# Performance work log

Hardware: AMD Instinct MI355X
Metric: run time of the kernel (lower is better)

## Reference

```python
import jax, jax.numpy as jnp
import numpy as np

H = 512  # hidden size (layer_size in the torch module)


def setup_inputs() -> dict:
    key = jax.random.key(0)
    ks = jax.random.split(key, 12)
    B, T = 512, 128
    s = 1.0 / np.sqrt(H)  # torch default LSTM/Linear init range
    def u(k, shape):
        return jax.random.uniform(k, shape, jnp.float32, -s, s)
    return {
        "x": jax.random.normal(ks[0], (B, T, 1), jnp.float32),
        "x_time": jax.random.normal(ks[1], (B, T), jnp.float32),
        "y_time": jax.random.normal(ks[2], (B, T), jnp.float32),
        # layer 0: input_size=1
        "w_ih0": u(ks[3], (4 * H, 1)),
        "w_hh0": u(ks[4], (4 * H, H)),
        "b_ih0": u(ks[5], (4 * H,)),
        "b_hh0": u(ks[6], (4 * H,)),
        # layer 1: input_size=H
        "w_ih1": u(ks[7], (4 * H, H)),
        "w_hh1": u(ks[8], (4 * H, H)),
        "b_ih1": u(ks[9], (4 * H,)),
        "b_hh1": u(ks[10], (4 * H,)),
        # output head Linear(512, 1)
        "w_lin": u(ks[11], (1, H)),
        "b_lin": jnp.zeros((1,), jnp.float32),
    }


def _cell(x, h, c, w_ih, w_hh, b):
    # torch LSTM gate order: i, f, g, o
    g = x @ w_ih.T + h @ w_hh.T + b
    i, f, gg, o = jnp.split(g, 4, axis=-1)
    c = jax.nn.sigmoid(f) * c + jax.nn.sigmoid(i) * jnp.tanh(gg)
    h = jax.nn.sigmoid(o) * jnp.tanh(c)
    return h, c


def reference(x, x_time, y_time, w_ih0, w_hh0, b_ih0, b_hh0,
              w_ih1, w_hh1, b_ih1, b_hh1, w_lin, b_lin):
    # x: [B, T, 1]; x_time / y_time are unused (as in the torch module)
    B, T, _ = x.shape
    b0 = b_ih0 + b_hh0
    b1 = b_ih1 + b_hh1

    def step(state, x_t):  # x_t: [B, 1]
        h1, c1, h2, c2 = state
        h1, c1 = _cell(x_t, h1, c1, w_ih0, w_hh0, b0)
        h2, c2 = _cell(h1, h2, c2, w_ih1, w_hh1, b1)
        return (h1, c1, h2, c2), h2

    z = jnp.zeros((B, H), x.dtype)
    state = (z, z, z, z)
    # phase 1: run the 2-layer LSTM over the full input sequence (first loop iter)
    state, _ = jax.lax.scan(step, state, jnp.swapaxes(x, 0, 1))
    y0 = state[3] @ w_lin.T + b_lin  # [B, 1] first prediction

    def ar_step(carry, _):
        st, y = carry
        st, h2 = step(st, y)
        y_new = h2 @ w_lin.T + b_lin
        return (st, y_new), y_new

    _, ys = jax.lax.scan(ar_step, (state, y0), None, length=T - 1)  # [T-1, B, 1]
    preds = jnp.concatenate([y0[None], ys], axis=0)  # [T, B, 1]
    return jnp.transpose(preds, (1, 0, 2))  # [B, T, 1]
```

## Files before the change

### kernel.cpp

```cpp
#include <hip/hip_runtime.h>
#include <math.h>
#include <stdint.h>


namespace {
constexpr int NH  = 512;
constexpr int NT  = 128;
constexpr int NB  = 512;
}

typedef __attribute__((ext_vector_type(8))) short bf16x8;
typedef __attribute__((ext_vector_type(4))) float f32x4;
typedef __attribute__((ext_vector_type(4))) unsigned int u32x4;

__global__ void ReLSTM_18940805775611_kernel() {}

__device__ __forceinline__ unsigned short lstm9_f2b(float f) {
    union { float f; uint32_t i; } v; v.f = f;
    const uint32_t r = v.i + 0x7FFFu + ((v.i >> 16) & 1u);
    return (unsigned short)(r >> 16);
}
__device__ __forceinline__ float lstm9_sig(float x) {
    return 1.0f / (1.0f + expf(-x));
}

__global__ void lstm9_mark(float* out) {
    const int i = blockIdx.x * blockDim.x + threadIdx.x;
    if (i < NB * NT) out[i] = 2.03125f;
}

__global__ void lstm9_prep(
    const float* whh0, const float* wih1, const float* whh1,
    const float* bih0, const float* bhh0, const float* bih1, const float* bhh1,
    unsigned short* wb0, unsigned short* wb1i, unsigned short* wb1h,
    float* bsum0, float* bsum1,
    unsigned short* hz, int* flags)
{
    const size_t stride = (size_t)gridDim.x * blockDim.x;
    const size_t i0 = (size_t)blockIdx.x * blockDim.x + threadIdx.x;
    const size_t NW = (size_t)4 * NH * NH;
    for (size_t i = i0; i < NW; i += stride) {
        wb0 [i] = lstm9_f2b(whh0[i]);
        wb1i[i] = lstm9_f2b(wih1[i]);
        wb1h[i] = lstm9_f2b(whh1[i]);
    }
    for (size_t i = i0; i < (size_t)4 * NH; i += stride) {
        bsum0[i] = bih0[i] + bhh0[i];
        bsum1[i] = bih1[i] + bhh1[i];
    }
    for (size_t i = i0; i < (size_t)4 * NB * NH; i += stride) hz[i] = 0;
    for (size_t i = i0; i < (size_t)2 * 256 * 8 * 32; i += stride) flags[i] = 0;
}

__device__ __forceinline__ void lstm9_ldA(u32x4& d, const unsigned short* p) {
    asm volatile("global_load_dwordx4 %0, %1, off sc0 sc1"
                 : "=v"(d) : "v"(p) : "memory");
}
__device__ __forceinline__ void lstm9_ldP(u32x4& d, const float* p) {
    asm volatile("global_load_dwordx4 %0, %1, off sc0 sc1"
                 : "=v"(d) : "v"(p) : "memory");
}
#define LSTM9_W8(N, a,b,c,d,e,f,g,h) \
    asm volatile("s_waitcnt vmcnt(" #N ")" \
        : "+v"(a),"+v"(b),"+v"(c),"+v"(d),"+v"(e),"+v"(f),"+v"(g),"+v"(h) :: "memory")
#define LSTM9_WAIT2(a,b) \
    asm volatile("s_waitcnt vmcnt(0)" : "+v"(a),"+v"(b) :: "memory")
__device__ __forceinline__ void lstm9_stH(unsigned short* p, unsigned short v) {
    unsigned int x = v;
    asm volatile("global_store_short %0, %1, off sc0 sc1" :: "v"(p), "v"(x) : "memory");
}
__device__ __forceinline__ void lstm9_stF(float* p, float v) {
    asm volatile("global_store_dword %0, %1, off sc0 sc1" :: "v"(p), "v"(v) : "memory");
}
__device__ __forceinline__ void lstm9_stI(int* p, int v) {
    asm volatile("global_store_dword %0, %1, off sc0 sc1" :: "v"(p), "v"(v) : "memory");
}
__device__ __forceinline__ void lstm9_drain() {
    asm volatile("s_waitcnt vmcnt(0)" ::: "memory");
}

__device__ __forceinline__ void lstm9_waitgrp(const int* base) {
    if (threadIdx.x < 64) {
        const int sl = (int)threadIdx.x & 31;
        int it = 0;
        for (;;) {
            int f;
            asm volatile("global_load_dword %0, %1, off sc0 sc1\n\t"
                         "s_waitcnt vmcnt(0)"
                         : "=v"(f) : "v"(base + sl) : "memory");
            if (__all(f != 0)) break;
            if (it < 4) __builtin_amdgcn_s_sleep(1);
            else        __builtin_amdgcn_s_sleep(8);
            ++it;
        }
    }
    __syncthreads();
}
__device__ __forceinline__ void lstm9_waitgrp2(const int* baseA, const int* baseB) {
    if (threadIdx.x < 64) {
        const int sl = (int)threadIdx.x & 31;
        const int* p = ((threadIdx.x < 32) ? baseA : baseB) + sl;
        int it = 0;
        for (;;) {
            int f;
            asm volatile("global_load_dword %0, %1, off sc0 sc1\n\t"
                         "s_waitcnt vmcnt(0)"
                         : "=v"(f) : "v"(p) : "memory");
            if (__all(f != 0)) break;
            if (it < 4) __builtin_amdgcn_s_sleep(1);
            else        __builtin_amdgcn_s_sleep(8);
            ++it;
        }
    }
    __syncthreads();
}

#define BFR0(gt, kk) (*(const bf16x8*)&Bsh0[gt][kk][lane][0])
#define BFR1(gt, kk) (*(const bf16x8*)&Bsh1[gt][kk][lane][0])
#define WHR(gt, kk)  (*(const bf16x8*)&whr[(gt) * 16 + (kk)])

#define LSTM9_L0_MFMAS()                                                          \
    do {                                                                          \
        _Pragma("unroll")                                                         \
        for (int ks = 0; ks < 8; ++ks) {                                          \
            const bf16x8 af = *(const bf16x8*)&rA1[ks];                           \
            b0 = __builtin_amdgcn_mfma_f32_16x16x32_bf16(af, BFR0(0, ks), b0, 0, 0, 0); \
            b1 = __builtin_amdgcn_mfma_f32_16x16x32_bf16(af, BFR0(1, ks), b1, 0, 0, 0); \
            b2 = __builtin_amdgcn_mfma_f32_16x16x32_bf16(af, BFR0(2, ks), b2, 0, 0, 0); \
            b3 = __builtin_amdgcn_mfma_f32_16x16x32_bf16(af, BFR0(3, ks), b3, 0, 0, 0); \
        }                                                                         \
        _Pragma("unroll")                                                         \
        for (int ks = 0; ks < 8; ++ks) {                                          \
            const bf16x8 af = *(const bf16x8*)&rA2[ks];                           \
            b0 = __builtin_amdgcn_mfma_f32_16x16x32_bf16(af, BFR0(0, 8 + ks), b0, 0, 0, 0); \
            b1 = __builtin_amdgcn_mfma_f32_16x16x32_bf16(af, BFR0(1, 8 + ks), b1, 0, 0, 0); \
            b2 = __builtin_amdgcn_mfma_f32_16x16x32_bf16(af, BFR0(2, 8 + ks), b2, 0, 0, 0); \
            b3 = __builtin_amdgcn_mfma_f32_16x16x32_bf16(af, BFR0(3, 8 + ks), b3, 0, 0, 0); \
        }                                                                         \
    } while (0)

#define LSTM9_L0_EPI(h1dst)                                                       \
    do {                                                                          \
        _Pragma("unroll")                                                         \
        for (int r = 0; r < 4; ++r) {                                             \
            const float gi = b0[r] + fmaf(xv[r], wxi, b0i);                       \
            const float gf = b1[r] + fmaf(xv[r], wxf, b0f);                       \
            const float gg = b2[r] + fmaf(xv[r], wxg, b0g);                       \
            const float go = b3[r] + fmaf(xv[r], wxo, b0o);                       \
            float cv = c1r[r];                                                    \
            cv = lstm9_sig(gf) * cv + lstm9_sig(gi) * tanhf(gg);                  \
            c1r[r] = cv;                                                          \
            lstm9_stH((h1dst) + (size_t)(mb + r) * NH + jv,                       \
                      lstm9_f2b(lstm9_sig(go) * tanhf(cv)));                      \
        }                                                                         \
    } while (0)

__global__ __launch_bounds__(256, 1) void lstm9_persist(
    const float* __restrict__ xin, float* __restrict__ outf,
    const unsigned short* __restrict__ wb0,
    const unsigned short* __restrict__ wb1i,
    const unsigned short* __restrict__ wb1h,
    const float* __restrict__ bsum0, const float* __restrict__ bsum1,
    const float* __restrict__ wih0f, const float* __restrict__ wlinf,
    const float* __restrict__ blinf,
    unsigned short* h1a, unsigned short* h1b,
    unsigned short* h2a, unsigned short* h2b,
    float* parts, int* flags)
{
    __shared__ unsigned short Bsh0[4][16][64][8];
    __shared__ unsigned short Bsh1[4][16][64][8];
    __shared__ float redsh[64][17];
    __shared__ float ysh[64];

    const int tid  = threadIdx.x;
    const int lane = tid & 63;
    const int wv   = tid >> 6;
    const int quad = lane >> 4;
    const int ln15 = lane & 15;
    const int bid  = blockIdx.x;
    const int jt = (bid & 7) * 4 + ((bid >> 3) & 3);
    const int g  = bid >> 5;
    const int j0 = jt * 16;
    const int m0 = g * 64;
    const int rowA = m0 + wv * 16 + ln15;
    const int mb   = m0 + wv * 16 + quad * 4;
    const int jv   = j0 + ln15;

    for (int idx = tid; idx < 4 * 16 * 64; idx += 256) {
        const int gt = idx >> 10;
        const int ks = (idx >> 6) & 15;
        const int l  = idx & 63;
        const int row = l & 15, q = l >> 4;
        const size_t go = ((size_t)(gt * NH + j0 + row)) * NH + ks * 32 + q * 8;
        *(u32x4*)&Bsh0[gt][ks][l][0] = *(const u32x4*)(wb0  + go);
        *(u32x4*)&Bsh1[gt][ks][l][0] = *(const u32x4*)(wb1i + go);
    }
    u32x4 whr[64];
    #pragma unroll
    for (int gt = 0; gt < 4; ++gt) {
        #pragma unroll
        for (int ks = 0; ks < 16; ++ks)
            whr[gt * 16 + ks] = *(const u32x4*)(
                wb1h + ((size_t)(gt * NH + j0 + ln15)) * NH + ks * 32 + quad * 8);
    }
    __syncthreads();

    const float b0i = bsum0[jv],          b0f = bsum0[NH + jv];
    const float b0g = bsum0[2 * NH + jv], b0o = bsum0[3 * NH + jv];
    const float wxi = wih0f[jv],          wxf = wih0f[NH + jv];
    const float wxg = wih0f[2 * NH + jv], wxo = wih0f[3 * NH + jv];
    const float b1i = bsum1[jv],          b1f = bsum1[NH + jv];
    const float b1g = bsum1[2 * NH + jv], b1o = bsum1[3 * NH + jv];
    const float wl_ = wlinf[jv];
    const float bl_ = blinf[0];

    float c1r[4] = {0.f, 0.f, 0.f, 0.f};
    float c2r[4] = {0.f, 0.f, 0.f, 0.f};

    unsigned short* h1p[2] = { h1a, h1b };
    unsigned short* h2p[2] = { h2a, h2b };
    int* flagA = flags;
    int* flagB = flags + 256 * 8 * 32;

    u32x4 rA1[8], rA2[8], rH2a[8], rH2b[8];

    {
        float xv[4];
        f32x4 b0 = {0.f, 0.f, 0.f, 0.f};
        f32x4 b1 = b0, b2 = b0, b3 = b0;
        #pragma unroll
        for (int r = 0; r < 4; ++r)
            xv[r] = xin[(size_t)(mb + r) * NT + 0];
        LSTM9_L0_EPI(h1p[1]);
        lstm9_drain();
        __syncthreads();
        if (tid == 0) lstm9_stI(flagA + (0 * 8 + g) * 32 + jt, 1);
    }

    for (int t = 0; t < 255; ++t) {
        const unsigned short* h1rd = h1p[(t + 1) & 1];
        unsigned short*       h1wr = h1p[t & 1];
        const unsigned short* h2rd = h2p[t & 1];
        unsigned short*       h2wr = h2p[(t + 1) & 1];

        if (t == 0) lstm9_waitgrp(flagA + (0 * 8 + g) * 32);
        else        lstm9_waitgrp2(flagA + (t * 8 + g) * 32,
                                   flagB + ((t - 1) * 8 + g) * 32);

        #pragma unroll
        for (int ks = 0; ks < 8; ++ks)
            lstm9_ldA(rH2a[ks], h2rd + (size_t)rowA * NH + ks * 32 + quad * 8);
        #pragma unroll
        for (int ks = 0; ks < 8; ++ks)
            lstm9_ldA(rH2b[ks], h2rd + (size_t)rowA * NH + (8 + ks) * 32 + quad * 8);
        #pragma unroll
        for (int ks = 0; ks < 8; ++ks)
            lstm9_ldA(rA1[ks], h1rd + (size_t)rowA * NH + ks * 32 + quad * 8);
        #pragma unroll
        for (int ks = 0; ks < 8; ++ks)
            lstm9_ldA(rA2[ks], h1rd + (size_t)rowA * NH + (8 + ks) * 32 + quad * 8);

        f32x4 a0 = {0.f, 0.f, 0.f, 0.f};
        f32x4 a1 = a0, a2 = a0, a3 = a0;
        LSTM9_W8(24, rH2a[0], rH2a[1], rH2a[2], rH2a[3],
                     rH2a[4], rH2a[5], rH2a[6], rH2a[7]);
        #pragma unroll
        for (int ks = 0; ks < 8; ++ks) {
            const bf16x8 af = *(const bf16x8*)&rH2a[ks];
            a0 = __builtin_amdgcn_mfma_f32_16x16x32_bf16(af, WHR(0, ks), a0, 0, 0, 0);
            a1 = __builtin_amdgcn_mfma_f32_16x16x32_bf16(af, WHR(1, ks), a1, 0, 0, 0);
            a2 = __builtin_amdgcn_mfma_f32_16x16x32_bf16(af, WHR(2, ks), a2, 0, 0, 0);
            a3 = __builtin_amdgcn_mfma_f32_16x16x32_bf16(af, WHR(3, ks), a3, 0, 0, 0);
        }
        LSTM9_W8(16, rH2b[0], rH2b[1], rH2b[2], rH2b[3],
                     rH2b[4], rH2b[5], rH2b[6], rH2b[7]);
        #pragma unroll
        for (int ks = 0; ks < 8; ++ks) {
            const bf16x8 af = *(const bf16x8*)&rH2b[ks];
            a0 = __builtin_amdgcn_mfma_f32_16x16x32_bf16(af, WHR(0, 8 + ks), a0, 0, 0, 0);
            a1 = __builtin_amdgcn_mfma_f32_16x16x32_bf16(af, WHR(1, 8 + ks), a1, 0, 0, 0);
            a2 = __builtin_amdgcn_mfma_f32_16x16x32_bf16(af, WHR(2, 8 + ks), a2, 0, 0, 0);
            a3 = __builtin_amdgcn_mfma_f32_16x16x32_bf16(af, WHR(3, 8 + ks), a3, 0, 0, 0);
        }
        LSTM9_W8(8, rA1[0], rA1[1], rA1[2], rA1[3],
                    rA1[4], rA1[5], rA1[6], rA1[7]);
        #pragma unroll
        for (int ks = 0; ks < 8; ++ks) {
            const bf16x8 af = *(const bf16x8*)&rA1[ks];
            a0 = __builtin_amdgcn_mfma_f32_16x16x32_bf16(af, BFR1(0, ks), a0, 0, 0, 0);
            a1 = __builtin_amdgcn_mfma_f32_16x16x32_bf16(af, BFR1(1, ks), a1, 0, 0, 0);
            a2 = __builtin_amdgcn_mfma_f32_16x16x32_bf16(af, BFR1(2, ks), a2, 0, 0, 0);
            a3 = __builtin_amdgcn_mfma_f32_16x16x32_bf16(af, BFR1(3, ks), a3, 0, 0, 0);
        }
        LSTM9_W8(0, rA2[0], rA2[1], rA2[2], rA2[3],
                    rA2[4], rA2[5], rA2[6], rA2[7]);
        #pragma unroll
        for (int ks = 0; ks < 8; ++ks) {
            const bf16x8 af = *(const bf16x8*)&rA2[ks];
            a0 = __builtin_amdgcn_mfma_f32_16x16x32_bf16(af, BFR1(0, 8 + ks), a0, 0, 0, 0);
            a1 = __builtin_amdgcn_mfma_f32_16x16x32_bf16(af, BFR1(1, 8 + ks), a1, 0, 0, 0);
            a2 = __builtin_amdgcn_mfma_f32_16x16x32_bf16(af, BFR1(2, 8 + ks), a2, 0, 0, 0);
            a3 = __builtin_amdgcn_mfma_f32_16x16x32_bf16(af, BFR1(3, 8 + ks), a3, 0, 0, 0);
        }

        float hv[4], cva[4];
        #pragma unroll
        for (int r = 0; r < 4; ++r) {
            const float gi = a0[r] + b1i;
            const float gf = a1[r] + b1f;
            const float gg = a2[r] + b1g;
            const float go = a3[r] + b1o;
            float cv = c2r[r];
            cv = lstm9_sig(gf) * cv + lstm9_sig(gi) * tanhf(gg);
            c2r[r] = cv;
            cva[r] = cv;
            hv[r] = lstm9_sig(go) * tanhf(cv);
            lstm9_stH(h2wr + (size_t)(mb + r) * NH + jv, lstm9_f2b(hv[r]));
        }

        f32x4 b0 = {0.f, 0.f, 0.f, 0.f};
        f32x4 b1 = b0, b2 = b0, b3 = b0;

        if (t < 127) {
            LSTM9_L0_MFMAS();
            float xv[4];
            #pragma unroll
            for (int r = 0; r < 4; ++r)
                xv[r] = xin[(size_t)(mb + r) * NT + (t + 1)];
            LSTM9_L0_EPI(h1wr);
            lstm9_drain();
            __syncthreads();
            if (tid == 0) {
                lstm9_stI(flagB + (t * 8 + g) * 32 + jt, 1);
                lstm9_stI(flagA + ((t + 1) * 8 + g) * 32 + jt, 1);
            }
        } else {
            #pragma unroll
            for (int r = 0; r < 4; ++r)
                redsh[wv * 16 + quad * 4 + r][ln15] =
                    (t == 127 ? cva[r] : hv[r]) * wl_;
            __syncthreads();
            if (tid < 64) {
                float s = 0.0f;
                #pragma unroll
                for (int j = 0; j < 16; ++j) s += redsh[tid][j];
                lstm9_stF(parts + (size_t)(t & 1) * NB * 32
                                + (size_t)(m0 + tid) * 32 + jt, s);
            }
            lstm9_drain();
            __syncthreads();
            if (tid == 0) lstm9_stI(flagB + (t * 8 + g) * 32 + jt, 1);

            if (t < 254) LSTM9_L0_MFMAS();

            lstm9_waitgrp(flagB + (t * 8 + g) * 32);
            const float* pslot = parts + (size_t)(t & 1) * NB * 32;
            {
                const int row = tid >> 2, q = tid & 3;
                u32x4 v0, v1;
                lstm9_ldP(v0, pslot + (size_t)(m0 + row) * 32 + q * 8);
                lstm9_ldP(v1, pslot + (size_t)(m0 + row) * 32 + q * 8 + 4);
                LSTM9_WAIT2(v0, v1);
                const float* f0 = (const float*)&v0;
                const float* f1 = (const float*)&v1;
                redsh[row][q] = f0[0] + f0[1] + f0[2] + f0[3]
                              + f1[0] + f1[1] + f1[2] + f1[3];
            }
            __syncthreads();
            if (tid < 64) {
                const float y = bl_ + redsh[tid][0] + redsh[tid][1]
                                    + redsh[tid][2] + redsh[tid][3];
                ysh[tid] = y;
                if (jt == 0)
                    outf[(size_t)(m0 + tid) * NT + (t - 127)] = y;
            }
            __syncthreads();
            if (t == 254) break;

            float xv[4];
            #pragma unroll
            for (int r = 0; r < 4; ++r)
                xv[r] = ysh[wv * 16 + quad * 4 + r];
            LSTM9_L0_EPI(h1wr);
            lstm9_drain();
            __syncthreads();
            if (tid == 0) lstm9_stI(flagA + ((t + 1) * 8 + g) * 32 + jt, 1);
        }
    }
}

extern "C" void kernel_launch(void* const* d_in, const int* in_sizes, int n_in,
                              void* d_out, int out_size, void* d_ws, size_t ws_size,
                              hipStream_t stream)
{
    int base = 3;
    if (!(n_in > 3 && in_sizes[3] == 4 * NH)) {
        for (int i = 1; i + 9 < n_in; ++i)
            if (in_sizes[i] == 4 * NH) { base = i; break; }
    }
    const float* xin  = (const float*)d_in[0];
    const float* wih0 = (const float*)d_in[base + 0];
    const float* whh0 = (const float*)d_in[base + 1];
    const float* bih0 = (const float*)d_in[base + 2];
    const float* bhh0 = (const float*)d_in[base + 3];
    const float* wih1 = (const float*)d_in[base + 4];
    const float* whh1 = (const float*)d_in[base + 5];
    const float* bih1 = (const float*)d_in[base + 6];
    const float* bhh1 = (const float*)d_in[base + 7];
    const float* wlin = (const float*)d_in[base + 8];
    const float* blin = (const float*)d_in[base + 9];
    float* outf = (float*)d_out;

    const size_t NW = (size_t)4 * NH * NH;
    const size_t S  = (size_t)NB * NH;
    unsigned short* wb0  = (unsigned short*)d_ws;
    unsigned short* wb1i = wb0 + NW;
    unsigned short* wb1h = wb1i + NW;
    unsigned short* h1b0 = wb1h + NW;
    unsigned short* h1b1 = h1b0 + S;
    unsigned short* h2b0 = h1b1 + S;
    unsigned short* h2b1 = h2b0 + S;
    float* bsum0 = (float*)(h2b1 + S);
    float* bsum1 = bsum0 + 4 * NH;
    float* parts = bsum1 + 4 * NH;
    int*   flags = (int*)(parts + 2 * NB * 32);

    lstm9_mark<<<(NB * NT + 255) / 256, 256, 0, stream>>>(outf);
    lstm9_prep<<<1024, 256, 0, stream>>>(whh0, wih1, whh1, bih0, bhh0, bih1, bhh1,
                                         wb0, wb1i, wb1h, bsum0, bsum1,
                                         h1b0, flags);
    lstm9_persist<<<256, 256, 0, stream>>>(xin, outf, wb0, wb1i, wb1h,
                                           bsum0, bsum1, wih0, wlin, blin,
                                           h1b0, h1b1, h2b0, h2b1,
                                           parts, flags);
}
```

Measured before the change: 3.076 ms.

## Restructure autoregressive phase to overlap layer-2 recurrent MFMAs with y reduction wait

Splits the main time loop into an encoder phase and an autoregressive phase. In the autoregressive phase it issues the h2 loads and the layer-0 MFMAs while the partial-sum loads for y are still in flight, then runs the h2·W_hh1 half of layer 1 before waiting for the new h1 from the other blocks. This hides part of the two grid-wide flag waits per step. The final y is reduced after the loop. Spin waits now use a fixed short sleep with a bounded retry count, which can fall through silently on timeout.

```diff
diff --git a/kernel.cpp b/kernel.cpp
--- a/kernel.cpp
+++ b/kernel.cpp
@@ -52,11 +52,7 @@
     for (size_t i = i0; i < (size_t)2 * 256 * 8 * 32; i += stride) flags[i] = 0;
 }
 
-__device__ __forceinline__ void lstm9_ldA(u32x4& d, const unsigned short* p) {
-    asm volatile("global_load_dwordx4 %0, %1, off sc0 sc1"
-                 : "=v"(d) : "v"(p) : "memory");
-}
-__device__ __forceinline__ void lstm9_ldP(u32x4& d, const float* p) {
+__device__ __forceinline__ void lstm9_ldA(u32x4& d, const void* p) {
     asm volatile("global_load_dwordx4 %0, %1, off sc0 sc1"
                  : "=v"(d) : "v"(p) : "memory");
 }
@@ -65,6 +61,8 @@
         : "+v"(a),"+v"(b),"+v"(c),"+v"(d),"+v"(e),"+v"(f),"+v"(g),"+v"(h) :: "memory")
 #define LSTM9_WAIT2(a,b) \
     asm volatile("s_waitcnt vmcnt(0)" : "+v"(a),"+v"(b) :: "memory")
+#define LSTM9_WP16(a,b) \
+    asm volatile("s_waitcnt vmcnt(16)" : "+v"(a),"+v"(b) :: "memory")
 __device__ __forceinline__ void lstm9_stH(unsigned short* p, unsigned short v) {
     unsigned int x = v;
     asm volatile("global_store_short %0, %1, off sc0 sc1" :: "v"(p), "v"(x) : "memory");
@@ -82,16 +80,15 @@
 __device__ __forceinline__ void lstm9_waitgrp(const int* base) {
     if (threadIdx.x < 64) {
         const int sl = (int)threadIdx.x & 31;
-        int it = 0;
+        int tries = 0;
         for (;;) {
             int f;
             asm volatile("global_load_dword %0, %1, off sc0 sc1\n\t"
                          "s_waitcnt vmcnt(0)"
                          : "=v"(f) : "v"(base + sl) : "memory");
             if (__all(f != 0)) break;
-            if (it < 4) __builtin_amdgcn_s_sleep(1);
-            else        __builtin_amdgcn_s_sleep(8);
-            ++it;
+            if (++tries > (1 << 15)) break;
+            __builtin_amdgcn_s_sleep(1);
         }
     }
     __syncthreads();
@@ -100,16 +97,15 @@
     if (threadIdx.x < 64) {
         const int sl = (int)threadIdx.x & 31;
         const int* p = ((threadIdx.x < 32) ? baseA : baseB) + sl;
-        int it = 0;
+        int tries = 0;
         for (;;) {
             int f;
             asm volatile("global_load_dword %0, %1, off sc0 sc1\n\t"
                          "s_waitcnt vmcnt(0)"
                          : "=v"(f) : "v"(p) : "memory");
             if (__all(f != 0)) break;
-            if (it < 4) __builtin_amdgcn_s_sleep(1);
-            else        __builtin_amdgcn_s_sleep(8);
-            ++it;
+            if (++tries > (1 << 15)) break;
+            __builtin_amdgcn_s_sleep(1);
         }
     }
     __syncthreads();
@@ -243,102 +239,222 @@
         const unsigned short* h2rd = h2p[t & 1];
         unsigned short*       h2wr = h2p[(t + 1) & 1];
 
-        if (t == 0) lstm9_waitgrp(flagA + (0 * 8 + g) * 32);
-        else        lstm9_waitgrp2(flagA + (t * 8 + g) * 32,
-                                   flagB + ((t - 1) * 8 + g) * 32);
-
-        #pragma unroll
-        for (int ks = 0; ks < 8; ++ks)
-            lstm9_ldA(rH2a[ks], h2rd + (size_t)rowA * NH + ks * 32 + quad * 8);
-        #pragma unroll
-        for (int ks = 0; ks < 8; ++ks)
-            lstm9_ldA(rH2b[ks], h2rd + (size_t)rowA * NH + (8 + ks) * 32 + quad * 8);
-        #pragma unroll
-        for (int ks = 0; ks < 8; ++ks)
-            lstm9_ldA(rA1[ks], h1rd + (size_t)rowA * NH + ks * 32 + quad * 8);
-        #pragma unroll
-        for (int ks = 0; ks < 8; ++ks)
-            lstm9_ldA(rA2[ks], h1rd + (size_t)rowA * NH + (8 + ks) * 32 + quad * 8);
-
-        f32x4 a0 = {0.f, 0.f, 0.f, 0.f};
-        f32x4 a1 = a0, a2 = a0, a3 = a0;
-        LSTM9_W8(24, rH2a[0], rH2a[1], rH2a[2], rH2a[3],
-                     rH2a[4], rH2a[5], rH2a[6], rH2a[7]);
-        #pragma unroll
-        for (int ks = 0; ks < 8; ++ks) {
-            const bf16x8 af = *(const bf16x8*)&rH2a[ks];
-            a0 = __builtin_amdgcn_mfma_f32_16x16x32_bf16(af, WHR(0, ks), a0, 0, 0, 0);
-            a1 = __builtin_amdgcn_mfma_f32_16x16x32_bf16(af, WHR(1, ks), a1, 0, 0, 0);
-            a2 = __builtin_amdgcn_mfma_f32_16x16x32_bf16(af, WHR(2, ks), a2, 0, 0, 0);
-            a3 = __builtin_amdgcn_mfma_f32_16x16x32_bf16(af, WHR(3, ks), a3, 0, 0, 0);
-        }
-        LSTM9_W8(16, rH2b[0], rH2b[1], rH2b[2], rH2b[3],
-                     rH2b[4], rH2b[5], rH2b[6], rH2b[7]);
-        #pragma unroll
-        for (int ks = 0; ks < 8; ++ks) {
-            const bf16x8 af = *(const bf16x8*)&rH2b[ks];
-            a0 = __builtin_amdgcn_mfma_f32_16x16x32_bf16(af, WHR(0, 8 + ks), a0, 0, 0, 0);
-            a1 = __builtin_amdgcn_mfma_f32_16x16x32_bf16(af, WHR(1, 8 + ks), a1, 0, 0, 0);
-            a2 = __builtin_amdgcn_mfma_f32_16x16x32_bf16(af, WHR(2, 8 + ks), a2, 0, 0, 0);
-            a3 = __builtin_amdgcn_mfma_f32_16x16x32_bf16(af, WHR(3, 8 + ks), a3, 0, 0, 0);
-        }
-        LSTM9_W8(8, rA1[0], rA1[1], rA1[2], rA1[3],
-                    rA1[4], rA1[5], rA1[6], rA1[7]);
-        #pragma unroll
-        for (int ks = 0; ks < 8; ++ks) {
-            const bf16x8 af = *(const bf16x8*)&rA1[ks];
-            a0 = __builtin_amdgcn_mfma_f32_16x16x32_bf16(af, BFR1(0, ks), a0, 0, 0, 0);
-            a1 = __builtin_amdgcn_mfma_f32_16x16x32_bf16(af, BFR1(1, ks), a1, 0, 0, 0);
-            a2 = __builtin_amdgcn_mfma_f32_16x16x32_bf16(af, BFR1(2, ks), a2, 0, 0, 0);
-            a3 = __builtin_amdgcn_mfma_f32_16x16x32_bf16(af, BFR1(3, ks), a3, 0, 0, 0);
-        }
-        LSTM9_W8(0, rA2[0], rA2[1], rA2[2], rA2[3],
-                    rA2[4], rA2[5], rA2[6], rA2[7]);
-        #pragma unroll
-        for (int ks = 0; ks < 8; ++ks) {
-            const bf16x8 af = *(const bf16x8*)&rA2[ks];
-            a0 = __builtin_amdgcn_mfma_f32_16x16x32_bf16(af, BFR1(0, 8 + ks), a0, 0, 0, 0);
-            a1 = __builtin_amdgcn_mfma_f32_16x16x32_bf16(af, BFR1(1, 8 + ks), a1, 0, 0, 0);
-            a2 = __builtin_amdgcn_mfma_f32_16x16x32_bf16(af, BFR1(2, 8 + ks), a2, 0, 0, 0);
-            a3 = __builtin_amdgcn_mfma_f32_16x16x32_bf16(af, BFR1(3, 8 + ks), a3, 0, 0, 0);
-        }
-
-        float hv[4], cva[4];
-        #pragma unroll
-        for (int r = 0; r < 4; ++r) {
-            const float gi = a0[r] + b1i;
-            const float gf = a1[r] + b1f;
-            const float gg = a2[r] + b1g;
-            const float go = a3[r] + b1o;
-            float cv = c2r[r];
-            cv = lstm9_sig(gf) * cv + lstm9_sig(gi) * tanhf(gg);
-            c2r[r] = cv;
-            cva[r] = cv;
-            hv[r] = lstm9_sig(go) * tanhf(cv);
-            lstm9_stH(h2wr + (size_t)(mb + r) * NH + jv, lstm9_f2b(hv[r]));
-        }
-
-        f32x4 b0 = {0.f, 0.f, 0.f, 0.f};
-        f32x4 b1 = b0, b2 = b0, b3 = b0;
-
-        if (t < 127) {
+        if (t <= 127) {
+            if (t == 0) lstm9_waitgrp(flagA + (0 * 8 + g) * 32);
+            else        lstm9_waitgrp2(flagA + (t * 8 + g) * 32,
+                                       flagB + ((t - 1) * 8 + g) * 32);
+
+            #pragma unroll
+            for (int ks = 0; ks < 8; ++ks)
+                lstm9_ldA(rH2a[ks], h2rd + (size_t)rowA * NH + ks * 32 + quad * 8);
+            #pragma unroll
+            for (int ks = 0; ks < 8; ++ks)
+                lstm9_ldA(rH2b[ks], h2rd + (size_t)rowA * NH + (8 + ks) * 32 + quad * 8);
+            #pragma unroll
+            for (int ks = 0; ks < 8; ++ks)
+                lstm9_ldA(rA1[ks], h1rd + (size_t)rowA * NH + ks * 32 + quad * 8);
+            #pragma unroll
+            for (int ks = 0; ks < 8; ++ks)
+                lstm9_ldA(rA2[ks], h1rd + (size_t)rowA * NH + (8 + ks) * 32 + quad * 8);
+
+            f32x4 a0 = {0.f, 0.f, 0.f, 0.f};
+            f32x4 a1 = a0, a2 = a0, a3 = a0;
+            LSTM9_W8(24, rH2a[0], rH2a[1], rH2a[2], rH2a[3],
+                         rH2a[4], rH2a[5], rH2a[6], rH2a[7]);
+            #pragma unroll
+            for (int ks = 0; ks < 8; ++ks) {
+                const bf16x8 af = *(const bf16x8*)&rH2a[ks];
+                a0 = __builtin_amdgcn_mfma_f32_16x16x32_bf16(af, WHR(0, ks), a0, 0, 0, 0);
+                a1 = __builtin_amdgcn_mfma_f32_16x16x32_bf16(af, WHR(1, ks), a1, 0, 0, 0);
+                a2 = __builtin_amdgcn_mfma_f32_16x16x32_bf16(af, WHR(2, ks), a2, 0, 0, 0);
+                a3 = __builtin_amdgcn_mfma_f32_16x16x32_bf16(af, WHR(3, ks), a3, 0, 0, 0);
+            }
+            LSTM9_W8(16, rH2b[0], rH2b[1], rH2b[2], rH2b[3],
+                         rH2b[4], rH2b[5], rH2b[6], rH2b[7]);
+            #pragma unroll
+            for (int ks = 0; ks < 8; ++ks) {
+                const bf16x8 af = *(const bf16x8*)&rH2b[ks];
+                a0 = __builtin_amdgcn_mfma_f32_16x16x32_bf16(af, WHR(0, 8 + ks), a0, 0, 0, 0);
+                a1 = __builtin_amdgcn_mfma_f32_16x16x32_bf16(af, WHR(1, 8 + ks), a1, 0, 0, 0);
+                a2 = __builtin_amdgcn_mfma_f32_16x16x32_bf16(af, WHR(2, 8 + ks), a2, 0, 0, 0);
+                a3 = __builtin_amdgcn_mfma_f32_16x16x32_bf16(af, WHR(3, 8 + ks), a3, 0, 0, 0);
+            }
+            LSTM9_W8(8, rA1[0], rA1[1], rA1[2], rA1[3],
+                        rA1[4], rA1[5], rA1[6], rA1[7]);
+            #pragma unroll
+            for (int ks = 0; ks < 8; ++ks) {
+                const bf16x8 af = *(const bf16x8*)&rA1[ks];
+                a0 = __builtin_amdgcn_mfma_f32_16x16x32_bf16(af, BFR1(0, ks), a0, 0, 0, 0);
+                a1 = __builtin_amdgcn_mfma_f32_16x16x32_bf16(af, BFR1(1, ks), a1, 0, 0, 0);
+                a2 = __builtin_amdgcn_mfma_f32_16x16x32_bf16(af, BFR1(2, ks), a2, 0, 0, 0);
+                a3 = __builtin_amdgcn_mfma_f32_16x16x32_bf16(af, BFR1(3, ks), a3, 0, 0, 0);
+            }
+            LSTM9_W8(0, rA2[0], rA2[1], rA2[2], rA2[3],
+                        rA2[4], rA2[5], rA2[6], rA2[7]);
+            #pragma unroll
+            for (int ks = 0; ks < 8; ++ks) {
+                const bf16x8 af = *(const bf16x8*)&rA2[ks];
+                a0 = __builtin_amdgcn_mfma_f32_16x16x32_bf16(af, BFR1(0, 8 + ks), a0, 0, 0, 0);
+                a1 = __builtin_amdgcn_mfma_f32_16x16x32_bf16(af, BFR1(1, 8 + ks), a1, 0, 0, 0);
+                a2 = __builtin_amdgcn_mfma_f32_16x16x32_bf16(af, BFR1(2, 8 + ks), a2, 0, 0, 0);
+                a3 = __builtin_amdgcn_mfma_f32_16x16x32_bf16(af, BFR1(3, 8 + ks), a3, 0, 0, 0);
+            }
+
+            float hv[4], cva[4];
+            #pragma unroll
+            for (int r = 0; r < 4; ++r) {
+                const float gi = a0[r] + b1i;
+                const float gf = a1[r] + b1f;
+                const float gg = a2[r] + b1g;
+                const float go = a3[r] + b1o;
+                float cv = c2r[r];
+                cv = lstm9_sig(gf) * cv + lstm9_sig(gi) * tanhf(gg);
+                c2r[r] = cv;
+                cva[r] = cv;
+                hv[r] = lstm9_sig(go) * tanhf(cv);
+                lstm9_stH(h2wr + (size_t)(mb + r) * NH + jv, lstm9_f2b(hv[r]));
+            }
+
+            f32x4 b0 = {0.f, 0.f, 0.f, 0.f};
+            f32x4 b1 = b0, b2 = b0, b3 = b0;
+
+            if (t < 127) {
+                LSTM9_L0_MFMAS();
+                float xv[4];
+                #pragma unroll
+                for (int r = 0; r < 4; ++r)
+                    xv[r] = xin[(size_t)(mb + r) * NT + (t + 1)];
+                LSTM9_L0_EPI(h1wr);
+                lstm9_drain();
+                __syncthreads();
+                if (tid == 0) {
+                    lstm9_stI(flagB + (t * 8 + g) * 32 + jt, 1);
+                    lstm9_stI(flagA + ((t + 1) * 8 + g) * 32 + jt, 1);
+                }
+            } else {
+                #pragma unroll
+                for (int r = 0; r < 4; ++r)
+                    redsh[wv * 16 + quad * 4 + r][ln15] = cva[r] * wl_;
+                __syncthreads();
+                if (tid < 64) {
+                    float s = 0.0f;
+                    #pragma unroll
+                    for (int j = 0; j < 16; ++j) s += redsh[tid][j];
+                    lstm9_stF(parts + (size_t)(127 & 1) * NB * 32
+                                    + (size_t)(m0 + tid) * 32 + jt, s);
+                }
+                lstm9_drain();
+                __syncthreads();
+                if (tid == 0) lstm9_stI(flagB + (127 * 8 + g) * 32 + jt, 1);
+            }
+        } else {
+            lstm9_waitgrp(flagB + ((t - 1) * 8 + g) * 32);
+
+            const float* pslot = parts + (size_t)((t - 1) & 1) * NB * 32;
+            const int prow = tid >> 2, pq = tid & 3;
+            u32x4 v0, v1;
+            lstm9_ldA(v0, pslot + (size_t)(m0 + prow) * 32 + pq * 8);
+            lstm9_ldA(v1, pslot + (size_t)(m0 + prow) * 32 + pq * 8 + 4);
+            #pragma unroll
+            for (int ks = 0; ks < 8; ++ks)
+                lstm9_ldA(rH2a[ks], h2rd + (size_t)rowA * NH + ks * 32 + quad * 8);
+            #pragma unroll
+            for (int ks = 0; ks < 8; ++ks)
+                lstm9_ldA(rH2b[ks], h2rd + (size_t)rowA * NH + (8 + ks) * 32 + quad * 8);
+
+            f32x4 b0 = {0.f, 0.f, 0.f, 0.f};
+            f32x4 b1 = b0, b2 = b0, b3 = b0;
             LSTM9_L0_MFMAS();
+
+            LSTM9_WP16(v0, v1);
+            {
+                const float* f0 = (const float*)&v0;
+                const float* f1 = (const float*)&v1;
+                redsh[prow][pq] = f0[0] + f0[1] + f0[2] + f0[3]
+                                + f1[0] + f1[1] + f1[2] + f1[3];
+            }
+            __syncthreads();
+            if (tid < 64) {
+                const float y = bl_ + redsh[tid][0] + redsh[tid][1]
+                                    + redsh[tid][2] + redsh[tid][3];
+                ysh[tid] = y;
+                if (jt == 0)
+                    outf[(size_t)(m0 + tid) * NT + (t - 128)] = y;
+            }
+            __syncthreads();
             float xv[4];
             #pragma unroll
             for (int r = 0; r < 4; ++r)
-                xv[r] = xin[(size_t)(mb + r) * NT + (t + 1)];
+                xv[r] = ysh[wv * 16 + quad * 4 + r];
+
             LSTM9_L0_EPI(h1wr);
             lstm9_drain();
             __syncthreads();
-            if (tid == 0) {
-                lstm9_stI(flagB + (t * 8 + g) * 32 + jt, 1);
-                lstm9_stI(flagA + ((t + 1) * 8 + g) * 32 + jt, 1);
-            }
-        } else {
+            if (tid == 0) lstm9_stI(flagA + (t * 8 + g) * 32 + jt, 1);
+
+            f32x4 a0 = {0.f, 0.f, 0.f, 0.f};
+            f32x4 a1 = a0, a2 = a0, a3 = a0;
+            #pragma unroll
+            for (int ks = 0; ks < 8; ++ks) {
+                const bf16x8 af = *(const bf16x8*)&rH2a[ks];
+                a0 = __builtin_amdgcn_mfma_f32_16x16x32_bf16(af, WHR(0, ks), a0, 0, 0, 0);
+                a1 = __builtin_amdgcn_mfma_f32_16x16x32_bf16(af, WHR(1, ks), a1, 0, 0, 0);
+                a2 = __builtin_amdgcn_mfma_f32_16x16x32_bf16(af, WHR(2, ks), a2, 0, 0, 0);
+                a3 = __builtin_amdgcn_mfma_f32_16x16x32_bf16(af, WHR(3, ks), a3, 0, 0, 0);
+            }
+            #pragma unroll
+            for (int ks = 0; ks < 8; ++ks) {
+                const bf16x8 af = *(const bf16x8*)&rH2b[ks];
+                a0 = __builtin_amdgcn_mfma_f32_16x16x32_bf16(af, WHR(0, 8 + ks), a0, 0, 0, 0);
+                a1 = __builtin_amdgcn_mfma_f32_16x16x32_bf16(af, WHR(1, 8 + ks), a1, 0, 0, 0);
+                a2 = __builtin_amdgcn_mfma_f32_16x16x32_bf16(af, WHR(2, 8 + ks), a2, 0, 0, 0);
+                a3 = __builtin_amdgcn_mfma_f32_16x16x32_bf16(af, WHR(3, 8 + ks), a3, 0, 0, 0);
+            }
+
+            lstm9_waitgrp(flagA + (t * 8 + g) * 32);
+            #pragma unroll
+            for (int ks = 0; ks < 8; ++ks)
+                lstm9_ldA(rA1[ks], h1wr + (size_t)rowA * NH + ks * 32 + quad * 8);
+            #pragma unroll
+            for (int ks = 0; ks < 8; ++ks)
+                lstm9_ldA(rA2[ks], h1wr + (size_t)rowA * NH + (8 + ks) * 32 + quad * 8);
+            LSTM9_W8(8, rA1[0], rA1[1], rA1[2], rA1[3],
+                        rA1[4], rA1[5], rA1[6], rA1[7]);
+            #pragma unroll
+            for (int ks = 0; ks < 8; ++ks) {
+                const bf16x8 af = *(const bf16x8*)&rA1[ks];
+                a0 = __builtin_amdgcn_mfma_f32_16x16x32_bf16(af, BFR1(0, ks), a0, 0, 0, 0);
+                a1 = __builtin_amdgcn_mfma_f32_16x16x32_bf16(af, BFR1(1, ks), a1, 0, 0, 0);
+                a2 = __builtin_amdgcn_mfma_f32_16x16x32_bf16(af, BFR1(2, ks), a2, 0, 0, 0);
+                a3 = __builtin_amdgcn_mfma_f32_16x16x32_bf16(af, BFR1(3, ks), a3, 0, 0, 0);
+            }
+            LSTM9_W8(0, rA2[0], rA2[1], rA2[2], rA2[3],
+                        rA2[4], rA2[5], rA2[6], rA2[7]);
+            #pragma unroll
+            for (int ks = 0; ks < 8; ++ks) {
+                const bf16x8 af = *(const bf16x8*)&rA2[ks];
+                a0 = __builtin_amdgcn_mfma_f32_16x16x32_bf16(af, BFR1(0, 8 + ks), a0, 0, 0, 0);
+                a1 = __builtin_amdgcn_mfma_f32_16x16x32_bf16(af, BFR1(1, 8 + ks), a1, 0, 0, 0);
+                a2 = __builtin_amdgcn_mfma_f32_16x16x32_bf16(af, BFR1(2, 8 + ks), a2, 0, 0, 0);
+                a3 = __builtin_amdgcn_mfma_f32_16x16x32_bf16(af, BFR1(3, 8 + ks), a3, 0, 0, 0);
+            }
+
+            float hv[4];
+            #pragma unroll
+            for (int r = 0; r < 4; ++r) {
+                const float gi = a0[r] + b1i;
+                const float gf = a1[r] + b1f;
+                const float gg = a2[r] + b1g;
+                const float go = a3[r] + b1o;
+                float cv = c2r[r];
+                cv = lstm9_sig(gf) * cv + lstm9_sig(gi) * tanhf(gg);
+                c2r[r] = cv;
+                hv[r] = lstm9_sig(go) * tanhf(cv);
+                lstm9_stH(h2wr + (size_t)(mb + r) * NH + jv, lstm9_f2b(hv[r]));
+            }
             #pragma unroll
             for (int r = 0; r < 4; ++r)
-                redsh[wv * 16 + quad * 4 + r][ln15] =
-                    (t == 127 ? cva[r] : hv[r]) * wl_;
+                redsh[wv * 16 + quad * 4 + r][ln15] = hv[r] * wl_;
             __syncthreads();
             if (tid < 64) {
                 float s = 0.0f;
@@ -350,42 +466,27 @@
             lstm9_drain();
             __syncthreads();
             if (tid == 0) lstm9_stI(flagB + (t * 8 + g) * 32 + jt, 1);
-
-            if (t < 254) LSTM9_L0_MFMAS();
-
-            lstm9_waitgrp(flagB + (t * 8 + g) * 32);
-            const float* pslot = parts + (size_t)(t & 1) * NB * 32;
-            {
-                const int row = tid >> 2, q = tid & 3;
-                u32x4 v0, v1;
-                lstm9_ldP(v0, pslot + (size_t)(m0 + row) * 32 + q * 8);
-                lstm9_ldP(v1, pslot + (size_t)(m0 + row) * 32 + q * 8 + 4);
-                LSTM9_WAIT2(v0, v1);
-                const float* f0 = (const float*)&v0;
-                const float* f1 = (const float*)&v1;
-                redsh[row][q] = f0[0] + f0[1] + f0[2] + f0[3]
-                              + f1[0] + f1[1] + f1[2] + f1[3];
-            }
-            __syncthreads();
-            if (tid < 64) {
-                const float y = bl_ + redsh[tid][0] + redsh[tid][1]
-                                    + redsh[tid][2] + redsh[tid][3];
-                ysh[tid] = y;
-                if (jt == 0)
-                    outf[(size_t)(m0 + tid) * NT + (t - 127)] = y;
-            }
-            __syncthreads();
-            if (t == 254) break;
-
-            float xv[4];
-            #pragma unroll
-            for (int r = 0; r < 4; ++r)
-                xv[r] = ysh[wv * 16 + quad * 4 + r];
-            LSTM9_L0_EPI(h1wr);
-            lstm9_drain();
-            __syncthreads();
-            if (tid == 0) lstm9_stI(flagA + ((t + 1) * 8 + g) * 32 + jt, 1);
         }
+    }
+
+    lstm9_waitgrp(flagB + (254 * 8 + g) * 32);
+    {
+        const float* pslot = parts + (size_t)(254 & 1) * NB * 32;
+        const int prow = tid >> 2, pq = tid & 3;
+        u32x4 v0, v1;
+        lstm9_ldA(v0, pslot + (size_t)(m0 + prow) * 32 + pq * 8);
+        lstm9_ldA(v1, pslot + (size_t)(m0 + prow) * 32 + pq * 8 + 4);
+        LSTM9_WAIT2(v0, v1);
+        const float* f0 = (const float*)&v0;
+        const float* f1 = (const float*)&v1;
+        redsh[prow][pq] = f0[0] + f0[1] + f0[2] + f0[3]
+                        + f1[0] + f1[1] + f1[2] + f1[3];
+    }
+    __syncthreads();
+    if (tid < 64 && jt == 0) {
+        const float y = bl_ + redsh[tid][0] + redsh[tid][1]
+                            + redsh[tid][2] + redsh[tid][3];
+        outf[(size_t)(m0 + tid) * NT + 127] = y;
     }
 }
 
```

New measurement: 3.030 ms. No clear change (-1.5%).
